# Kernel optimization log

Measured on AMD Instinct MI355X. Metric: run time of the kernel, lower is better.

The kernel has to match this reference:

```python
import jax, jax.numpy as jnp
import numpy as np

B, C_CLS, D_WORD, J = 1024, 80, 300, 8000
IMG_CH = 2048

def setup_inputs() -> dict:
    key = jax.random.key(0)
    ks = jax.random.split(key, 9)
    return {
        'feature': jax.random.normal(ks[0], (B, IMG_CH), jnp.float32),
        'inp': jax.random.normal(ks[1], (1, C_CLS, D_WORD), jnp.float32),
        'A': jax.random.uniform(ks[2], (C_CLS, C_CLS), jnp.float32),
        'W_gc1': jax.random.normal(ks[3], (D_WORD, 1024), jnp.float32) * (1.0 / np.sqrt(1024)),
        'W_gc2': jax.random.normal(ks[4], (1024, 2048), jnp.float32) * (1.0 / np.sqrt(2048)),
        'W_img': jax.random.normal(ks[5], (J, IMG_CH), jnp.float32) * 0.02,
        'b_img': jax.random.normal(ks[6], (J,), jnp.float32) * 0.02,
        'W_cls': jax.random.normal(ks[7], (J, 2048), jnp.float32) * 0.02,
        'b_cls': jax.random.normal(ks[8], (J,), jnp.float32) * 0.02,
    }

def _gen_adj(A):
    # torch: D = A.sum(1)**-0.5; adj = (A @ diag(D)).T @ diag(D) = D[:,None]*A.T*D[None,:]
    D = jnp.power(jnp.sum(A, axis=1), -0.5)
    return D[:, None] * A.T * D[None, :]

def reference(feature, inp, A, W_gc1, W_gc2, W_img, b_img, W_cls, b_cls):
    inp0 = inp[0]                                   # [C, 300]
    adj = jax.lax.stop_gradient(_gen_adj(A))        # [C, C], .detach() in torch
    x = adj @ (inp0 @ W_gc1)                        # gc1: [C, 1024]
    x = jax.nn.leaky_relu(x, negative_slope=0.2)
    x = adj @ (x @ W_gc2)                           # gc2: [C, 2048]
    # MFB bilinear pooling (is_usemfb=True, is_hash=False -> out_in_tmp=1, eval-mode dropout=identity)
    # original: out[b,c] = sum_j (Linear_img(feature[b])[j] * Linear_cls(x_col_c)[j])
    img_proj = feature @ W_img.T + b_img            # [B, J]
    cls_proj = x @ W_cls.T + b_cls                  # [C, J]
    x_out = img_proj @ cls_proj.T                   # [B, C]
    return x_out
```

## Files before the change

### kernel.cpp

```cpp
#include <hip/hip_runtime.h>
#include <hip/hip_bf16.h>


typedef __bf16 bf16_t;
typedef __bf16 bf16x8 __attribute__((ext_vector_type(8)));
typedef float f32x4 __attribute__((ext_vector_type(4)));

#define MFMA16(a, b, c) __builtin_amdgcn_mfma_f32_16x16x32_bf16((a), (b), (c), 0, 0, 0)

#define GLOAD_LDS16(g, l)                                     \
  __builtin_amdgcn_global_load_lds(                           \
      (const __attribute__((address_space(1))) void*)(g),     \
      (__attribute__((address_space(3))) void*)(l), 16, 0, 0)

#define PIN()                                   \
  do {                                          \
    asm volatile("" ::: "memory");              \
    __builtin_amdgcn_sched_barrier(0);          \
  } while (0)

__device__ inline bf16x8 cvt8(float4 a, float4 b) {
  bf16x8 v;
  v[0] = (bf16_t)a.x; v[1] = (bf16_t)a.y; v[2] = (bf16_t)a.z; v[3] = (bf16_t)a.w;
  v[4] = (bf16_t)b.x; v[5] = (bf16_t)b.y; v[6] = (bf16_t)b.z; v[7] = (bf16_t)b.w;
  return v;
}

__global__ __launch_bounds__(256) void k_prep(
    const float* __restrict__ A, const float* __restrict__ inp0,
    float* __restrict__ adj, bf16_t* __restrict__ x0b,
    float* __restrict__ t2, float* __restrict__ H,
    float* __restrict__ r, float* __restrict__ out) {
  int b = blockIdx.x, tid = threadIdx.x;
  if (b == 0) {
    __shared__ float Dv[80];
    if (tid < 80) {
      float s = 0.f;
      #pragma unroll 4
      for (int j = 0; j < 80; ++j) s += A[tid * 80 + j];
      Dv[tid] = rsqrtf(s);
    }
    __syncthreads();
    for (int idx = tid; idx < 6400; idx += 256) {
      int i = idx / 80, j = idx % 80;
      adj[idx] = Dv[i] * Dv[j] * A[j * 80 + i];
    }
  } else if (b <= 120) {
    int idx = (b - 1) * 256 + tid;
    if (idx < 30720) {
      int c = idx / 384, k = idx % 384;
      x0b[idx] = (k < 300) ? (bf16_t)inp0[c * 300 + k] : (bf16_t)0.f;
    }
  } else {
    int t = (b - 121) * 256 + tid;
    const int NT = 39 * 256;
    float4 z = make_float4(0.f, 0.f, 0.f, 0.f);
    for (int i = t; i < 40960; i += NT) ((float4*)t2)[i] = z;
    for (int i = t; i < 40960; i += NT) ((float4*)H)[i] = z;
    for (int i = t; i < 20480; i += NT) ((float4*)out)[i] = z;
    if (t < 20) ((float4*)r)[t] = z;
  }
}

__global__ __launch_bounds__(256) void k_gc1m(
    const bf16_t* __restrict__ x0b, const float* __restrict__ Wgc1,
    float* __restrict__ t1) {
  int tid = threadIdx.x;
  int w = tid >> 6, l = tid & 63;
  int ln = l & 15, q = l >> 4;
  int n0 = blockIdx.x * 16;

  __shared__ float red[4][80][16];
  f32x4 acc[5] = {};
  for (int ks = 0; ks < 3; ++ks) {
    int kq = w * 96 + ks * 32 + q * 8;
    bf16x8 bfrag;
    #pragma unroll
    for (int jj = 0; jj < 8; ++jj) {
      int k = kq + jj;
      int kc = k < 300 ? k : 299;
      float wv = Wgc1[kc * 1024 + n0 + ln];
      bfrag[jj] = (bf16_t)(k < 300 ? wv : 0.f);
    }
    #pragma unroll
    for (int mt = 0; mt < 5; ++mt) {
      bf16x8 afrag = *(const bf16x8*)(x0b + (size_t)(mt * 16 + ln) * 384 + kq);
      acc[mt] = MFMA16(afrag, bfrag, acc[mt]);
    }
  }
  #pragma unroll
  for (int mt = 0; mt < 5; ++mt)
    #pragma unroll
    for (int reg = 0; reg < 4; ++reg)
      red[w][mt * 16 + q * 4 + reg][ln] = acc[mt][reg];
  __syncthreads();
  for (int o = tid; o < 1280; o += 256) {
    int c = o >> 4, nn = o & 15;
    t1[c * 1024 + n0 + nn] = red[0][c][nn] + red[1][c][nn] + red[2][c][nn] + red[3][c][nn];
  }
}

__global__ void k_adjmul_leaky(const float* __restrict__ adj, const float* __restrict__ t1,
                               bf16_t* __restrict__ x1b) {
  int idx = blockIdx.x * blockDim.x + threadIdx.x;
  int c = idx >> 10, n = idx & 1023;
  const float* ar = adj + c * 80;
  float acc = 0.f;
  #pragma unroll 4
  for (int cc = 0; cc < 80; ++cc) acc += ar[cc] * t1[cc * 1024 + n];
  x1b[idx] = (bf16_t)(acc > 0.f ? acc : 0.2f * acc);
}

__global__ __launch_bounds__(256) void k_gc2m(
    const bf16_t* __restrict__ x1b, const float* __restrict__ Wgc2,
    float* __restrict__ t2) {
  int tid = threadIdx.x;
  int w = tid >> 6, l = tid & 63;
  int ln = l & 15, q = l >> 4;
  int nc = blockIdx.x & 31, kc = blockIdx.x >> 5;

  __shared__ float BsF[2 * 2048];
  auto stage = [&](int b, int k0) {
    #pragma unroll
    for (int it = 0; it < 2; ++it) {
      int slot = tid + it * 256;
      int kr = slot >> 4, nq = slot & 15;
      const float* src = Wgc2 + (size_t)(k0 + kr) * 2048 + nc * 64 + nq * 4;
      float* dst = BsF + b * 2048 + slot * 4;
      GLOAD_LDS16(src, dst);
    }
  };

  int kb = kc * 64;
  bf16x8 a0[5], a1[5];
  #pragma unroll
  for (int mt = 0; mt < 5; ++mt)
    a0[mt] = *(const bf16x8*)(x1b + (size_t)(mt * 16 + ln) * 1024 + kb + q * 8);
  PIN();
  stage(0, kb);
  PIN();
  stage(1, kb + 32);
  PIN();
  #pragma unroll
  for (int mt = 0; mt < 5; ++mt)
    a1[mt] = *(const bf16x8*)(x1b + (size_t)(mt * 16 + ln) * 1024 + kb + 32 + q * 8);
  PIN();

  f32x4 acc[5] = {};
  asm volatile("s_waitcnt vmcnt(7)" ::: "memory");
  PIN();
  __builtin_amdgcn_s_barrier();
  PIN();
  {
    bf16x8 bfrag;
    #pragma unroll
    for (int jj = 0; jj < 8; ++jj) bfrag[jj] = (bf16_t)BsF[(q * 8 + jj) * 64 + w * 16 + ln];
    #pragma unroll
    for (int mt = 0; mt < 5; ++mt) acc[mt] = MFMA16(a0[mt], bfrag, acc[mt]);
  }
  asm volatile("s_waitcnt vmcnt(5)" ::: "memory");
  PIN();
  __builtin_amdgcn_s_barrier();
  PIN();
  {
    bf16x8 bfrag;
    #pragma unroll
    for (int jj = 0; jj < 8; ++jj)
      bfrag[jj] = (bf16_t)BsF[2048 + (q * 8 + jj) * 64 + w * 16 + ln];
    #pragma unroll
    for (int mt = 0; mt < 5; ++mt) acc[mt] = MFMA16(a1[mt], bfrag, acc[mt]);
  }

  #pragma unroll
  for (int mt = 0; mt < 5; ++mt)
    #pragma unroll
    for (int reg = 0; reg < 4; ++reg)
      atomicAdd(&t2[(size_t)(mt * 16 + q * 4 + reg) * 2048 + nc * 64 + w * 16 + ln],
                acc[mt][reg]);
}

__global__ void k_adjmul_bf16(const float* __restrict__ adj, const float* __restrict__ t2,
                              bf16_t* __restrict__ x2) {
  int idx = blockIdx.x * blockDim.x + threadIdx.x;
  int c = idx >> 11, n = idx & 2047;
  const float* ar = adj + c * 80;
  float acc = 0.f;
  #pragma unroll 4
  for (int cc = 0; cc < 80; ++cc) acc += ar[cc] * t2[cc * 2048 + n];
  x2[idx] = (bf16_t)acc;
}

__global__ __launch_bounds__(256) void k_clsproj(
    const float* __restrict__ Wcls, const float* __restrict__ bcls,
    const float* __restrict__ bimg, const bf16_t* __restrict__ x2,
    bf16_t* __restrict__ P, float* __restrict__ r) {
  int tid = threadIdx.x;
  int w = tid >> 6, l = tid & 63;
  int ln = l & 15, q = l >> 4;
  int j0 = blockIdx.x * 16;
  size_t jrow = (size_t)(j0 + ln) * 2048;

  __shared__ float red[4][80][16];
  __shared__ float rloc[80];
  if (tid < 80) rloc[tid] = 0.f;

  f32x4 acc[5] = {};
  int kbase = w * 512 + q * 8;
  for (int ks = 0; ks < 16; ++ks) {
    int kq = kbase + ks * 32;
    const float4* bp = (const float4*)(Wcls + jrow + kq);
    float4 b0 = bp[0], b1 = bp[1];
    bf16x8 bfrag = cvt8(b0, b1);
    #pragma unroll
    for (int mt = 0; mt < 5; ++mt) {
      bf16x8 afrag = *(const bf16x8*)(x2 + (size_t)(mt * 16 + ln) * 2048 + kq);
      acc[mt] = MFMA16(afrag, bfrag, acc[mt]);
    }
  }
  #pragma unroll
  for (int mt = 0; mt < 5; ++mt)
    #pragma unroll
    for (int reg = 0; reg < 4; ++reg)
      red[w][mt * 16 + q * 4 + reg][ln] = acc[mt][reg];
  __syncthreads();

  for (int o = tid; o < 1280; o += 256) {
    int c = o >> 4, jj = o & 15;
    float v = red[0][c][jj] + red[1][c][jj] + red[2][c][jj] + red[3][c][jj] + bcls[j0 + jj];
    P[(size_t)c * 8000 + j0 + jj] = (bf16_t)v;
    atomicAdd(&rloc[c], bimg[j0 + jj] * v);
  }
  __syncthreads();
  if (tid < 80) atomicAdd(&r[tid], rloc[tid]);
}

__global__ __launch_bounds__(256) void k_hmat(
    const float* __restrict__ Wimg, const bf16_t* __restrict__ P, float* __restrict__ H) {
  int tid = threadIdx.x;
  int w = tid >> 6, l = tid & 63;
  int ln = l & 15, q = l >> 4;
  int jc = blockIdx.x >> 4, ncg = blockIdx.x & 15;
  int jbase = jc * 320;
  int n0 = (ncg * 4 + w) * 32;

  __shared__ float Bs[4 * 3 * 1024];
  float* Bw = Bs + w * 3072;

  auto stage = [&](int buf, int jt) {
    #pragma unroll
    for (int it = 0; it < 4; ++it) {
      int row = it * 8 + (l >> 3);
      const float* src = Wimg + (size_t)(jt + row) * 2048 + n0 + (l & 7) * 4;
      float* dst = Bw + buf * 1024 + it * 256 + l * 4;
      GLOAD_LDS16(src, dst);
    }
  };
  auto loadA = [&](bf16x8* a, int j0) {
    #pragma unroll
    for (int mt = 0; mt < 5; ++mt)
      a[mt] = *(const bf16x8*)(P + (size_t)(mt * 16 + ln) * 8000 + j0 + q * 8);
  };

  f32x4 acc[5][2] = {};
  bf16x8 aCur[5], aNxt[5];

  loadA(aCur, jbase);
  PIN();
  stage(0, jbase);
  PIN();
  stage(1, jbase + 32);
  PIN();

  #pragma unroll
  for (int s = 0; s < 10; ++s) {
    if (s < 9) {
      loadA(aNxt, jbase + (s + 1) * 32);
      PIN();
    }
    if (s < 8) {
      stage((s + 2) % 3, jbase + (s + 2) * 32);
      PIN();
    }
    if (s < 8)       asm volatile("s_waitcnt vmcnt(13)" ::: "memory");
    else if (s == 8) asm volatile("s_waitcnt vmcnt(9)"  ::: "memory");
    else             asm volatile("s_waitcnt vmcnt(5)"  ::: "memory");
    PIN();
    const float* Bc = Bw + (s % 3) * 1024;
    bf16x8 bfrag[2];
    #pragma unroll
    for (int nt = 0; nt < 2; ++nt)
      #pragma unroll
      for (int jj = 0; jj < 8; ++jj)
        bfrag[nt][jj] = (bf16_t)Bc[(q * 8 + jj) * 32 + nt * 16 + ln];
    #pragma unroll
    for (int mt = 0; mt < 5; ++mt)
      #pragma unroll
      for (int nt = 0; nt < 2; ++nt)
        acc[mt][nt] = MFMA16(aCur[mt], bfrag[nt], acc[mt][nt]);
    PIN();
    if (s < 9) {
      #pragma unroll
      for (int mt = 0; mt < 5; ++mt) aCur[mt] = aNxt[mt];
    }
  }

  #pragma unroll
  for (int mt = 0; mt < 5; ++mt)
    #pragma unroll
    for (int nt = 0; nt < 2; ++nt)
      #pragma unroll
      for (int reg = 0; reg < 4; ++reg)
        atomicAdd(&H[(size_t)(mt * 16 + q * 4 + reg) * 2048 + n0 + nt * 16 + ln],
                  acc[mt][nt][reg]);
}

__global__ __launch_bounds__(256) void k_out(
    const float* __restrict__ feat, const float* __restrict__ H,
    const float* __restrict__ r, float* __restrict__ out) {
  int tid = threadIdx.x;
  int w = tid >> 6, l = tid & 63;
  int ln = l & 15, q = l >> 4;
  int mg = blockIdx.x & 15, kc = blockIdx.x >> 4;
  int m0 = mg * 64 + w * 16;
  size_t frow = (size_t)(m0 + ln) * 2048;

  f32x4 acc[5] = {};
  int kbase = kc * 64 + q * 8;
  #pragma unroll
  for (int ks = 0; ks < 2; ++ks) {
    int kq = kbase + ks * 32;
    const float4* ap = (const float4*)(feat + frow + kq);
    bf16x8 afrag = cvt8(ap[0], ap[1]);
    #pragma unroll
    for (int nt = 0; nt < 5; ++nt) {
      const float4* hp = (const float4*)(H + (size_t)(nt * 16 + ln) * 2048 + kq);
      bf16x8 bfrag = cvt8(hp[0], hp[1]);
      acc[nt] = MFMA16(afrag, bfrag, acc[nt]);
    }
  }
  #pragma unroll
  for (int nt = 0; nt < 5; ++nt)
    #pragma unroll
    for (int reg = 0; reg < 4; ++reg) {
      int b = m0 + q * 4 + reg;
      int c = nt * 16 + ln;
      float v = acc[nt][reg];
      if (kc == 0) v += r[c];
      atomicAdd(&out[b * 80 + c], v);
    }
}

extern "C" void kernel_launch(void* const* d_in, const int* in_sizes, int n_in,
                              void* d_out, int out_size, void* d_ws, size_t ws_size,
                              hipStream_t stream) {
  const float* feature = (const float*)d_in[0];
  const float* inp     = (const float*)d_in[1];
  const float* A       = (const float*)d_in[2];
  const float* Wgc1    = (const float*)d_in[3];
  const float* Wgc2    = (const float*)d_in[4];
  const float* Wimg    = (const float*)d_in[5];
  const float* bimg    = (const float*)d_in[6];
  const float* Wcls    = (const float*)d_in[7];
  const float* bcls    = (const float*)d_in[8];
  float* out = (float*)d_out;

  char* ws = (char*)d_ws;
  float*  adj = (float*)(ws + 0);
  float*  t1  = (float*)(ws + 25600);
  bf16_t* x1b = (bf16_t*)(ws + 353280);
  float*  t2  = (float*)(ws + 517120);
  bf16_t* x2  = (bf16_t*)(ws + 1172480);
  bf16_t* P   = (bf16_t*)(ws + 1500160);
  float*  H   = (float*)(ws + 2780160);
  float*  r   = (float*)(ws + 3435520);
  bf16_t* x0b = (bf16_t*)(ws + 3435840);

  k_prep<<<160, 256, 0, stream>>>(A, inp, adj, x0b, t2, H, r, out);
  k_gc1m<<<64, 256, 0, stream>>>(x0b, Wgc1, t1);
  k_adjmul_leaky<<<320, 256, 0, stream>>>(adj, t1, x1b);
  k_gc2m<<<512, 256, 0, stream>>>(x1b, Wgc2, t2);
  k_adjmul_bf16<<<640, 256, 0, stream>>>(adj, t2, x2);
  k_clsproj<<<500, 256, 0, stream>>>(Wcls, bcls, bimg, x2, P, r);
  k_hmat<<<400, 256, 0, stream>>>(Wimg, P, H);
  k_out<<<512, 256, 0, stream>>>(feature, H, r, out);
}
```

Measured before the change: 256.5 us.

## Split cls-proj reduction over K into four blocks with fp32 atomic partials

The cls projection kernel now splits its 2048-long reduction across four blocks per 16-column tile (2000 blocks instead of 500), accumulating fp32 partials into a zeroed temporary buffer with atomics. A new finalize kernel converts the partials to bf16 and computes the bias-image dot products. The aim is to fill more compute units on the weight-streaming stage, at the cost of an extra 5 MB zero-fill, atomic traffic and one more launch. The H-matrix kernel also replaces the register copy of A fragments with ping-pong indexing, and its final waitcnt now waits for all loads.

```diff
diff --git a/kernel.cpp b/kernel.cpp
--- a/kernel.cpp
+++ b/kernel.cpp
@@ -30,7 +30,7 @@
     const float* __restrict__ A, const float* __restrict__ inp0,
     float* __restrict__ adj, bf16_t* __restrict__ x0b,
     float* __restrict__ t2, float* __restrict__ H,
-    float* __restrict__ r, float* __restrict__ out) {
+    float* __restrict__ Ptmp, float* __restrict__ r, float* __restrict__ out) {
   int b = blockIdx.x, tid = threadIdx.x;
   if (b == 0) {
     __shared__ float Dv[80];
@@ -53,11 +53,12 @@
     }
   } else {
     int t = (b - 121) * 256 + tid;
-    const int NT = 39 * 256;
+    const int NT = 79 * 256;
     float4 z = make_float4(0.f, 0.f, 0.f, 0.f);
     for (int i = t; i < 40960; i += NT) ((float4*)t2)[i] = z;
     for (int i = t; i < 40960; i += NT) ((float4*)H)[i] = z;
     for (int i = t; i < 20480; i += NT) ((float4*)out)[i] = z;
+    for (int i = t; i < 160000; i += NT) ((float4*)Ptmp)[i] = z;
     if (t < 20) ((float4*)r)[t] = z;
   }
 }
@@ -192,21 +193,19 @@
 
 __global__ __launch_bounds__(256) void k_clsproj(
     const float* __restrict__ Wcls, const float* __restrict__ bcls,
-    const float* __restrict__ bimg, const bf16_t* __restrict__ x2,
-    bf16_t* __restrict__ P, float* __restrict__ r) {
+    const bf16_t* __restrict__ x2, float* __restrict__ Ptmp) {
   int tid = threadIdx.x;
   int w = tid >> 6, l = tid & 63;
   int ln = l & 15, q = l >> 4;
-  int j0 = blockIdx.x * 16;
+  int kc = blockIdx.x & 3;
+  int j0 = (blockIdx.x >> 2) * 16;
   size_t jrow = (size_t)(j0 + ln) * 2048;
 
   __shared__ float red[4][80][16];
-  __shared__ float rloc[80];
-  if (tid < 80) rloc[tid] = 0.f;
-
   f32x4 acc[5] = {};
-  int kbase = w * 512 + q * 8;
-  for (int ks = 0; ks < 16; ++ks) {
+  int kbase = kc * 512 + w * 128 + q * 8;
+  #pragma unroll
+  for (int ks = 0; ks < 4; ++ks) {
     int kq = kbase + ks * 32;
     const float4* bp = (const float4*)(Wcls + jrow + kq);
     float4 b0 = bp[0], b1 = bp[1];
@@ -226,9 +225,26 @@
 
   for (int o = tid; o < 1280; o += 256) {
     int c = o >> 4, jj = o & 15;
-    float v = red[0][c][jj] + red[1][c][jj] + red[2][c][jj] + red[3][c][jj] + bcls[j0 + jj];
-    P[(size_t)c * 8000 + j0 + jj] = (bf16_t)v;
-    atomicAdd(&rloc[c], bimg[j0 + jj] * v);
+    float v = red[0][c][jj] + red[1][c][jj] + red[2][c][jj] + red[3][c][jj];
+    if (kc == 0) v += bcls[j0 + jj];
+    atomicAdd(&Ptmp[(size_t)c * 8000 + j0 + jj], v);
+  }
+}
+
+__global__ __launch_bounds__(256) void k_pfin(
+    const float* __restrict__ Ptmp, const float* __restrict__ bimg,
+    bf16_t* __restrict__ P, float* __restrict__ r) {
+  __shared__ float rloc[80];
+  int tid = threadIdx.x;
+  if (tid < 80) rloc[tid] = 0.f;
+  __syncthreads();
+  for (int i = blockIdx.x * 256 + tid; i < 160000; i += 200 * 256) {
+    int c = i / 2000, jq = i % 2000;
+    float4 v = ((const float4*)Ptmp)[i];
+    float4 b = ((const float4*)bimg)[jq];
+    bf16_t p4[4] = {(bf16_t)v.x, (bf16_t)v.y, (bf16_t)v.z, (bf16_t)v.w};
+    __builtin_memcpy(P + (size_t)c * 8000 + jq * 4, p4, 8);
+    atomicAdd(&rloc[c], v.x * b.x + v.y * b.y + v.z * b.z + v.w * b.w);
   }
   __syncthreads();
   if (tid < 80) atomicAdd(&r[tid], rloc[tid]);
@@ -262,9 +278,9 @@
   };
 
   f32x4 acc[5][2] = {};
-  bf16x8 aCur[5], aNxt[5];
-
-  loadA(aCur, jbase);
+  bf16x8 aF[2][5];
+
+  loadA(aF[0], jbase);
   PIN();
   stage(0, jbase);
   PIN();
@@ -274,7 +290,7 @@
   #pragma unroll
   for (int s = 0; s < 10; ++s) {
     if (s < 9) {
-      loadA(aNxt, jbase + (s + 1) * 32);
+      loadA(aF[(s + 1) & 1], jbase + (s + 1) * 32);
       PIN();
     }
     if (s < 8) {
@@ -283,7 +299,7 @@
     }
     if (s < 8)       asm volatile("s_waitcnt vmcnt(13)" ::: "memory");
     else if (s == 8) asm volatile("s_waitcnt vmcnt(9)"  ::: "memory");
-    else             asm volatile("s_waitcnt vmcnt(5)"  ::: "memory");
+    else             asm volatile("s_waitcnt vmcnt(0)"  ::: "memory");
     PIN();
     const float* Bc = Bw + (s % 3) * 1024;
     bf16x8 bfrag[2];
@@ -296,12 +312,8 @@
     for (int mt = 0; mt < 5; ++mt)
       #pragma unroll
       for (int nt = 0; nt < 2; ++nt)
-        acc[mt][nt] = MFMA16(aCur[mt], bfrag[nt], acc[mt][nt]);
+        acc[mt][nt] = MFMA16(aF[s & 1][mt], bfrag[nt], acc[mt][nt]);
     PIN();
-    if (s < 9) {
-      #pragma unroll
-      for (int mt = 0; mt < 5; ++mt) aCur[mt] = aNxt[mt];
-    }
   }
 
   #pragma unroll
@@ -365,22 +377,24 @@
   float* out = (float*)d_out;
 
   char* ws = (char*)d_ws;
-  float*  adj = (float*)(ws + 0);
-  float*  t1  = (float*)(ws + 25600);
-  bf16_t* x1b = (bf16_t*)(ws + 353280);
-  float*  t2  = (float*)(ws + 517120);
-  bf16_t* x2  = (bf16_t*)(ws + 1172480);
-  bf16_t* P   = (bf16_t*)(ws + 1500160);
-  float*  H   = (float*)(ws + 2780160);
-  float*  r   = (float*)(ws + 3435520);
-  bf16_t* x0b = (bf16_t*)(ws + 3435840);
-
-  k_prep<<<160, 256, 0, stream>>>(A, inp, adj, x0b, t2, H, r, out);
+  float*  adj  = (float*)(ws + 0);
+  float*  t1   = (float*)(ws + 25600);
+  bf16_t* x1b  = (bf16_t*)(ws + 353280);
+  float*  t2   = (float*)(ws + 517120);
+  bf16_t* x2   = (bf16_t*)(ws + 1172480);
+  bf16_t* P    = (bf16_t*)(ws + 1500160);
+  float*  H    = (float*)(ws + 2780160);
+  float*  r    = (float*)(ws + 3435520);
+  bf16_t* x0b  = (bf16_t*)(ws + 3435840);
+  float*  Ptmp = (float*)(ws + 3497280);
+
+  k_prep<<<200, 256, 0, stream>>>(A, inp, adj, x0b, t2, H, Ptmp, r, out);
   k_gc1m<<<64, 256, 0, stream>>>(x0b, Wgc1, t1);
   k_adjmul_leaky<<<320, 256, 0, stream>>>(adj, t1, x1b);
   k_gc2m<<<512, 256, 0, stream>>>(x1b, Wgc2, t2);
   k_adjmul_bf16<<<640, 256, 0, stream>>>(adj, t2, x2);
-  k_clsproj<<<500, 256, 0, stream>>>(Wcls, bcls, bimg, x2, P, r);
+  k_clsproj<<<2000, 256, 0, stream>>>(Wcls, bcls, x2, Ptmp);
+  k_pfin<<<200, 256, 0, stream>>>(Ptmp, bimg, P, r);
   k_hmat<<<400, 256, 0, stream>>>(Wimg, P, H);
   k_out<<<512, 256, 0, stream>>>(feature, H, r, out);
 }
```

Measured after the change: 265.2 us. +3.4%, slower.
